# Kernel tuning notes

Hardware: AMD Instinct MI355X
Metric: run time of the kernel (lower is better)

Reference implementation:

```python
import jax, jax.numpy as jnp
import numpy as np
from jax import lax

DETER, STOCH, UNITS, ADIM, EMBED = 4096, 512, 1024, 2, 4096
B, T = 16, 64
ACTION_CLIP = 1.0


def setup_inputs() -> dict:
    key = jax.random.key(0)
    ks = jax.random.split(key, 16)
    s = 0.02
    f32 = jnp.float32
    return {
        "embed": jax.random.normal(ks[0], (B, T, EMBED), f32),
        "action": jax.random.normal(ks[1], (B, T, ADIM), f32),
        "is_first": jax.random.randint(ks[2], (B, T), 0, 2).astype(jnp.int32),
        # learned initial deter state
        "initial_deter": jnp.zeros((DETER,), f32),
        # obs_out: Linear(deter+4096 -> units)
        "w_obs": (jax.random.normal(ks[3], (UNITS, DETER + EMBED), f32) * s),
        "b_obs": jnp.zeros((UNITS,), f32),
        # img_in: Linear(stoch+action_dim -> units)
        "w_imgin": (jax.random.normal(ks[4], (UNITS, STOCH + ADIM), f32) * s),
        "b_imgin": jnp.zeros((UNITS,), f32),
        # img_out: Linear(deter -> units)
        "w_imgout": (jax.random.normal(ks[5], (UNITS, DETER), f32) * s),
        "b_imgout": jnp.zeros((UNITS,), f32),
        # GRUCell params (torch layout: [3*hidden, in] with r,z,n gate order)
        "w_ih": (jax.random.normal(ks[6], (3 * DETER, UNITS), f32) * s),
        "w_hh": (jax.random.normal(ks[7], (3 * DETER, DETER), f32) * s),
        "b_ih": jnp.zeros((3 * DETER,), f32),
        "b_hh": jnp.zeros((3 * DETER,), f32),
        # reparameterization noise for prior/post rsample at each step
        "eps_prior": jax.random.normal(ks[8], (T, B, STOCH), f32),
        "eps_post": jax.random.normal(ks[9], (T, B, STOCH), f32),
    }


def _stats(x):
    mean, std = jnp.split(x, 2, axis=-1)
    std = 2.0 * jax.nn.sigmoid(std / 2.0) + 0.1
    return mean, jnp.maximum(std, 1e-4)  # clamp from get_dist


def _gru(x, h, w_ih, w_hh, b_ih, b_hh):
    gi = x @ w_ih.T + b_ih  # [B, 3*deter]
    gh = h @ w_hh.T + b_hh
    ir, iz, inn = jnp.split(gi, 3, axis=-1)
    hr, hz, hn = jnp.split(gh, 3, axis=-1)
    r = jax.nn.sigmoid(ir + hr)
    z = jax.nn.sigmoid(iz + hz)
    n = jnp.tanh(inn + r * hn)
    return (1.0 - z) * n + z * h


def reference(embed, action, is_first, initial_deter, w_obs, b_obs,
              w_imgin, b_imgin, w_imgout, b_imgout,
              w_ih, w_hh, b_ih, b_hh, eps_prior, eps_post):
    bsz = action.shape[0]
    # initial_state (learned)
    deter0 = jnp.broadcast_to(jnp.tanh(initial_deter)[None, :], (bsz, DETER))
    m0, _ = _stats(deter0 @ w_imgout.T + b_imgout)
    stoch0 = m0  # dist.mean

    def step(carry, xs):
        deter, stoch = carry
        a, emb, first, ep, eo = xs  # [B,A], [B,E], [B], [B,S], [B,S]
        # action clip
        a = a * (ACTION_CLIP / jnp.maximum(jnp.abs(a), ACTION_CLIP))
        mask = (1.0 - first.astype(jnp.float32))[:, None]
        deter_m = deter * mask
        stoch_m = stoch * mask
        a = a * mask
        # img_step
        x = jnp.concatenate([stoch_m, a], axis=-1) @ w_imgin.T + b_imgin
        d_new = _gru(x, deter_m, w_ih, w_hh, b_ih, b_hh)
        pmean, pstd = _stats(d_new @ w_imgout.T + b_imgout)
        pstoch = pmean + pstd * ep
        # obs part
        z = jnp.concatenate([d_new, emb], axis=-1) @ w_obs.T + b_obs
        omean, ostd = _stats(z)
        ostoch = omean + ostd * eo
        out = jnp.concatenate(
            [ostoch, omean, ostd, d_new, pstoch, pmean, pstd, d_new], axis=-1)
        return (d_new, ostoch), out

    xs = (jnp.swapaxes(action, 0, 1), jnp.swapaxes(embed, 0, 1),
          jnp.swapaxes(is_first, 0, 1), eps_prior, eps_post)
    _, outs = lax.scan(step, (deter0, stoch0), xs)  # [T, B, F]
    return jnp.swapaxes(outs, 0, 1)  # [B, T, F]
```

## Files before the change

### kernel.cpp

```cpp
#include <hip/hip_runtime.h>
#include <math.h>

#define B_ 16
#define T_ 64
#define DETER_ 4096
#define STOCH_ 512
#define UNITS_ 1024
#define EMBED_ 4096
#define FOUT_ 11264

enum { JOB_IMGIN=0, JOB_GATES=1, JOB_PRIOR=2, JOB_OBS=3, JOB_PRIOR_INIT=4 };

struct SP {
  const float* embed; const float* action; const int* is_first;
  const float* wpad_imgin; const float* b_imgin;
  const float* w_ih; const float* w_hh; const float* b_ih; const float* b_hh;
  const float* w_imgout; const float* b_imgout;
  const float* w_obs; const float* b_obs;
  const float* eps_prior; const float* eps_post;
  const float* deter_m_in;
  float*       deter_m_out;
  float*       dnew;
  float* stoch_m; float* x_img; float* out;
  int t;
};

__device__ __forceinline__ float4 ld4(const float* p){ return *reinterpret_cast<const float4*>(p); }
__device__ __forceinline__ float sigm(float x){ return 1.f/(1.f+expf(-x)); }
__device__ __forceinline__ float dot4(float4 w, float4 x, float a){
  return fmaf(w.x,x.x, fmaf(w.y,x.y, fmaf(w.z,x.z, fmaf(w.w,x.w, a))));
}

__device__ __forceinline__ void g2l16(const float* g, float* l) {
  __builtin_amdgcn_global_load_lds(
      (const __attribute__((address_space(1))) unsigned int*)g,
      (__attribute__((address_space(3))) unsigned int*)l, 16, 0, 0);
}

__global__ __launch_bounds__(512,4) void gates_pipe(SP p) {
  __shared__ float Xs[16384];
  const int bid = blockIdx.x;
  const int tid = threadIdx.x;
  const int wave = tid>>6, lane = tid&63;
  const int half = lane>>5, sl = lane&31;
  const int t = p.t;
  const int j = bid*8 + wave;
  float* buf0 = Xs; float* buf1 = Xs + 8192;

  float ar[8], az[8], anx[8], anh[8];
  #pragma unroll
  for (int b=0;b<8;++b){ ar[b]=0.f; az[b]=0.f; anx[b]=0.f; anh[b]=0.f; }

  auto stage = [&](float* dst, int c) {
    #pragma unroll
    for (int q=0;q<2;++q) {
      const int b = wave*2+q;
      const float* src = (c<2) ? (p.x_img + b*UNITS_ + c*512)
                               : (p.deter_m_in + b*DETER_ + (c-2)*512);
      g2l16(src + lane*4,       dst + b*512);
      g2l16(src + 256 + lane*4, dst + b*512 + 256);
    }
  };

#define GINNER(AN)                                                      \
  _Pragma("unroll")                                                     \
  for (int it=0; it<4; ++it) {                                          \
    const int k0 = it*128 + sl*4;                                       \
    float4 w_r = ld4(wr+k0), w_z = ld4(wz+k0), w_n = ld4(wn+k0);        \
    _Pragma("unroll")                                                   \
    for (int b=0;b<8;++b) {                                             \
      float4 xv = ld4(cur + (half*8+b)*512 + k0);                       \
      ar[b] = dot4(w_r, xv, ar[b]);                                     \
      az[b] = dot4(w_z, xv, az[b]);                                     \
      AN[b] = dot4(w_n, xv, AN[b]);                                     \
    }                                                                   \
  }

  stage(buf0, 0);
  for (int c=0;c<10;++c) {
    float* cur = (c&1)? buf1 : buf0;
    float* nxt = (c&1)? buf0 : buf1;
    __builtin_amdgcn_s_barrier();
    __builtin_amdgcn_sched_barrier(0);
    if (c < 9) {
      stage(nxt, c+1);
      __builtin_amdgcn_sched_barrier(0);
      asm volatile("s_waitcnt vmcnt(4)" ::: "memory");
    } else {
      asm volatile("s_waitcnt vmcnt(0)" ::: "memory");
    }
    __builtin_amdgcn_sched_barrier(0);
    __builtin_amdgcn_s_barrier();

    const float *wr, *wz, *wn;
    if (c < 2) {
      const size_t o = (size_t)c*512;
      wr = p.w_ih + (size_t)j*1024 + o;
      wz = p.w_ih + (size_t)(4096+j)*1024 + o;
      wn = p.w_ih + (size_t)(8192+j)*1024 + o;
      GINNER(anx)
    } else {
      const size_t o = (size_t)(c-2)*512;
      wr = p.w_hh + (size_t)j*4096 + o;
      wz = p.w_hh + (size_t)(4096+j)*4096 + o;
      wn = p.w_hh + (size_t)(8192+j)*4096 + o;
      GINNER(anh)
    }
  }
#undef GINNER

  #pragma unroll
  for (int off=1; off<32; off<<=1) {
    #pragma unroll
    for (int b=0;b<8;++b) {
      ar[b]  += __shfl_xor(ar[b],  off);
      az[b]  += __shfl_xor(az[b],  off);
      anx[b] += __shfl_xor(anx[b], off);
      anh[b] += __shfl_xor(anh[b], off);
    }
  }
  if (sl==0) {
    #pragma unroll
    for (int b=0;b<8;++b) {
      buf0[(wave*4+0)*16 + half*8 + b] = ar[b];
      buf0[(wave*4+1)*16 + half*8 + b] = az[b];
      buf0[(wave*4+2)*16 + half*8 + b] = anx[b];
      buf0[(wave*4+3)*16 + half*8 + b] = anh[b];
    }
  }
  __syncthreads();

  if (tid < 128) {
    int u = tid&7, b = tid>>3;
    int jj = bid*8 + u;
    const float* res = Xs;
    float rs = res[(u*4+0)*16+b] + p.b_ih[jj]          + p.b_hh[jj];
    float zs = res[(u*4+1)*16+b] + p.b_ih[DETER_+jj]   + p.b_hh[DETER_+jj];
    float ni = res[(u*4+2)*16+b] + p.b_ih[2*DETER_+jj];
    float nh = res[(u*4+3)*16+b] + p.b_hh[2*DETER_+jj];
    float rg = sigm(rs), zg = sigm(zs);
    float ng = tanhf(ni + rg*nh);
    float hp = p.deter_m_in[b*DETER_+jj];
    float d  = (1.f-zg)*ng + zg*hp;
    p.dnew[b*DETER_+jj] = d;
    int tn = t+1;
    float mb2 = (tn<T_) ? (p.is_first[b*T_+tn] ? 0.f : 1.f) : 0.f;
    p.deter_m_out[b*DETER_+jj] = d*mb2;
    size_t ob = ((size_t)(b*T_+t))*FOUT_;
    p.out[ob+1536+jj] = d;
    p.out[ob+7168+jj] = d;
  }
}

template<int JOB>
__device__ __forceinline__ void pipe_mv(const SP& p, int bid, float* Xs) {
  constexpr int NC = (JOB==JOB_OBS)?16:8;
  const int tid = threadIdx.x;
  const int wave = tid>>6, lane = tid&63;
  const int half = lane>>5, sl = lane&31;
  const int t = p.t;
  float* buf0 = Xs; float* buf1 = Xs + 8192;

  float acc[2][8];
  #pragma unroll
  for (int r=0;r<2;++r)
    #pragma unroll
    for (int b=0;b<8;++b) acc[r][b]=0.f;

  int row0, row1;
  {
    int rl0 = wave*2, rl1 = wave*2+1;
    row0 = (rl0<4)? (bid*4+rl0) : (512 + bid*4 + (rl0-4));
    row1 = (rl1<4)? (bid*4+rl1) : (512 + bid*4 + (rl1-4));
  }

  auto stage = [&](float* dst, int c) {
    #pragma unroll
    for (int q=0;q<4;++q) {
      const int b = wave*4+q;
      const float* src;
      if constexpr (JOB==JOB_PRIOR) src = p.dnew + b*DETER_ + c*512;
      else src = (c<8) ? (p.dnew + b*DETER_ + c*512)
                       : (p.embed + ((size_t)(b*T_+t))*EMBED_ + (c-8)*512);
      g2l16(src + lane*4,       dst + b*512);
      g2l16(src + 256 + lane*4, dst + b*512 + 256);
    }
  };

  stage(buf0, 0);
  for (int c=0;c<NC;++c) {
    float* cur = (c&1)? buf1 : buf0;
    float* nxt = (c&1)? buf0 : buf1;
    __builtin_amdgcn_s_barrier();
    __builtin_amdgcn_sched_barrier(0);
    if (c+1 < NC) {
      stage(nxt, c+1);
      __builtin_amdgcn_sched_barrier(0);
      asm volatile("s_waitcnt vmcnt(8)" ::: "memory");
    } else {
      asm volatile("s_waitcnt vmcnt(0)" ::: "memory");
    }
    __builtin_amdgcn_sched_barrier(0);
    __builtin_amdgcn_s_barrier();

    const float *w0, *w1;
    if constexpr (JOB==JOB_PRIOR) {
      w0 = p.w_imgout + (size_t)row0*4096 + (size_t)c*512;
      w1 = p.w_imgout + (size_t)row1*4096 + (size_t)c*512;
    } else {
      w0 = p.w_obs + (size_t)row0*8192 + (size_t)c*512;
      w1 = p.w_obs + (size_t)row1*8192 + (size_t)c*512;
    }
    #pragma unroll
    for (int it=0; it<4; ++it) {
      const int k0 = it*128 + sl*4;
      float4 wa = ld4(w0+k0), wb2 = ld4(w1+k0);
      #pragma unroll
      for (int b=0;b<8;++b) {
        float4 xv = ld4(cur + (half*8+b)*512 + k0);
        acc[0][b] = dot4(wa,  xv, acc[0][b]);
        acc[1][b] = dot4(wb2, xv, acc[1][b]);
      }
    }
  }

  #pragma unroll
  for (int off=1; off<32; off<<=1)
    #pragma unroll
    for (int r=0;r<2;++r)
      #pragma unroll
      for (int b=0;b<8;++b)
        acc[r][b] += __shfl_xor(acc[r][b], off);
  if (sl==0) {
    #pragma unroll
    for (int r=0;r<2;++r)
      #pragma unroll
      for (int b=0;b<8;++b)
        buf0[(wave*2+r)*16 + half*8 + b] = acc[r][b];
  }
  __syncthreads();
  const float* res = Xs;

  if constexpr (JOB==JOB_PRIOR) {
    if (tid < 64) {
      int rl = tid&3, b = tid>>2;
      int jj = bid*4 + rl;
      float mean = res[rl*16+b]     + p.b_imgout[jj];
      float sr   = res[(rl+4)*16+b] + p.b_imgout[512+jj];
      float sd = 2.f*sigm(sr*0.5f) + 0.1f; sd = fmaxf(sd, 1e-4f);
      float ep = p.eps_prior[((size_t)t*B_+b)*STOCH_ + jj];
      size_t ob = ((size_t)(b*T_+t))*FOUT_;
      p.out[ob+5632+jj] = fmaf(sd, ep, mean);
      p.out[ob+6144+jj] = mean;
      p.out[ob+6656+jj] = sd;
    }
  } else {
    if (tid < 64) {
      int rl = tid&3, b = tid>>2;
      int jj = bid*4 + rl;
      float mean = res[rl*16+b]     + p.b_obs[jj];
      float sr   = res[(rl+4)*16+b] + p.b_obs[512+jj];
      float sd = 2.f*sigm(sr*0.5f) + 0.1f; sd = fmaxf(sd, 1e-4f);
      float eo = p.eps_post[((size_t)t*B_+b)*STOCH_ + jj];
      float ost = fmaf(sd, eo, mean);
      size_t ob = ((size_t)(b*T_+t))*FOUT_;
      p.out[ob+0+jj]    = ost;
      p.out[ob+512+jj]  = mean;
      p.out[ob+1024+jj] = sd;
      int tn = t+1;
      float mb2 = (tn<T_) ? (p.is_first[b*T_+tn] ? 0.f : 1.f) : 0.f;
      p.stoch_m[b*STOCH_+jj] = ost*mb2;
    }
  }
}

__global__ __launch_bounds__(256,2) void post_pipe(SP p) {
  __shared__ float Xs[16384];
  if (blockIdx.x < 128) pipe_mv<JOB_PRIOR>(p, blockIdx.x, Xs);
  else                  pipe_mv<JOB_OBS>(p, blockIdx.x - 128, Xs);
}

template<int JOB>
__device__ __forceinline__ void stage_async(const SP& p, float* Xs, int c,
                                            int wave, int lane, int tid, int t) {
  __syncthreads();
  constexpr int SEGS = (JOB==JOB_IMGIN) ? 2 : 4;
  #pragma unroll
  for (int q=0;q<4;++q) {
    const int b = wave*4+q;
    const float* src;
    if constexpr (JOB==JOB_PRIOR_INIT)
      src = p.dnew + b*DETER_ + c*1024;
    else
      src = p.stoch_m + b*STOCH_;
    float* dst = Xs + b*1024;
    #pragma unroll
    for (int seg=0;seg<SEGS;++seg)
      g2l16(src + seg*256 + lane*4, dst + seg*256);
  }
  if constexpr (JOB==JOB_IMGIN) {
    const int kc = tid*4;
    if (kc >= 512) {
      #pragma unroll
      for (int b=0;b<16;++b) {
        float4 v = make_float4(0.f,0.f,0.f,0.f);
        if (kc == 512) {
          float mb = p.is_first[b*T_+t] ? 0.f : 1.f;
          const float* ap = p.action + (b*T_+t)*2;
          float a0 = ap[0], a1 = ap[1];
          v.x = (a0 / fmaxf(fabsf(a0),1.f))*mb;
          v.y = (a1 / fmaxf(fabsf(a1),1.f))*mb;
        }
        *reinterpret_cast<float4*>(Xs + b*1024 + kc) = v;
      }
    }
  }
  __syncthreads();
}

template<int JOB>
__device__ __forceinline__ void mv_body(const SP& p, int bid, float* Xs) {
  constexpr int KTOT = (JOB==JOB_IMGIN)?1024:4096;
  constexpr int CHUNKS = KTOT/1024;
  const int tid = threadIdx.x;
  const int wave = tid>>6, lane = tid&63;
  const int half = lane>>5, sl = lane&31;
  const int t = p.t;

  float acc[2][8];
  #pragma unroll
  for (int r=0;r<2;++r)
    #pragma unroll
    for (int b=0;b<8;++b) acc[r][b]=0.f;

  int rowIdx[2];
  #pragma unroll
  for (int r=0;r<2;++r) rowIdx[r] = bid*8 + wave*2 + r;

  for (int c=0;c<CHUNKS;++c) {
    stage_async<JOB>(p, Xs, c, wave, lane, tid, t);
    const float* w0; const float* w1;
    if constexpr (JOB==JOB_IMGIN) {
      w0 = p.wpad_imgin + (size_t)rowIdx[0]*1024;
      w1 = p.wpad_imgin + (size_t)rowIdx[1]*1024;
    } else {
      w0 = p.w_imgout + (size_t)rowIdx[0]*4096 + (size_t)c*1024;
      w1 = p.w_imgout + (size_t)rowIdx[1]*4096 + (size_t)c*1024;
    }
    #pragma unroll
    for (int it=0; it<8; ++it) {
      const int k0 = it*128 + sl*4;
      float4 wa = ld4(w0 + k0), wb2 = ld4(w1 + k0);
      #pragma unroll
      for (int b=0;b<8;++b) {
        float4 xv = ld4(Xs + (half*8+b)*1024 + k0);
        acc[0][b] = dot4(wa,  xv, acc[0][b]);
        acc[1][b] = dot4(wb2, xv, acc[1][b]);
      }
    }
  }

  #pragma unroll
  for (int off=1; off<32; off<<=1)
    #pragma unroll
    for (int r=0;r<2;++r)
      #pragma unroll
      for (int b=0;b<8;++b)
        acc[r][b] += __shfl_xor(acc[r][b], off);
  __syncthreads();
  if (sl==0) {
    #pragma unroll
    for (int r=0;r<2;++r)
      #pragma unroll
      for (int b=0;b<8;++b)
        Xs[(wave*2+r)*16 + half*8 + b] = acc[r][b];
  }
  __syncthreads();
  const float* res = Xs;

  if constexpr (JOB==JOB_IMGIN) {
    if (tid < 128) {
      int rl = tid&7, b = tid>>3;
      int row = bid*8 + rl;
      p.x_img[b*UNITS_+row] = res[rl*16+b] + p.b_imgin[row];
    }
  } else {
    if (tid < 128) {
      int rl = tid&7, b = tid>>3;
      int row = bid*8 + rl;
      float mean = res[rl*16+b] + p.b_imgout[row];
      float mb = p.is_first[b*T_+0] ? 0.f : 1.f;
      p.stoch_m[b*STOCH_+row] = mean*mb;
    }
  }
}

template<int JOB>
__global__ __launch_bounds__(256,2) void mv_single(SP p) {
  __shared__ float Xs[16*1024];
  mv_body<JOB>(p, blockIdx.x, Xs);
}

__global__ void pad_imgin_kernel(const float* w, float* wpad) {
  int row = blockIdx.x;
  for (int k=threadIdx.x; k<1024; k+=256)
    wpad[row*1024+k] = (k<514) ? w[row*514+k] : 0.f;
}

__global__ void init_deter_kernel(const float* ini, float* det, float* detm,
                                  const int* is_first) {
  int k = blockIdx.x*256 + threadIdx.x;
  float v = tanhf(ini[k]);
  #pragma unroll
  for (int b=0;b<16;++b) {
    det[b*DETER_+k] = v;
    float mb = is_first[b*T_+0] ? 0.f : 1.f;
    detm[b*DETER_+k] = v*mb;
  }
}

extern "C" void kernel_launch(void* const* d_in, const int* in_sizes, int n_in,
                              void* d_out, int out_size, void* d_ws, size_t ws_size,
                              hipStream_t stream) {
  (void)in_sizes; (void)n_in; (void)out_size; (void)ws_size;
  SP p;
  p.embed     = (const float*)d_in[0];
  p.action    = (const float*)d_in[1];
  p.is_first  = (const int*)  d_in[2];
  const float* initial_deter = (const float*)d_in[3];
  p.w_obs     = (const float*)d_in[4];
  p.b_obs     = (const float*)d_in[5];
  const float* w_imgin       = (const float*)d_in[6];
  p.b_imgin   = (const float*)d_in[7];
  p.w_imgout  = (const float*)d_in[8];
  p.b_imgout  = (const float*)d_in[9];
  p.w_ih      = (const float*)d_in[10];
  p.w_hh      = (const float*)d_in[11];
  p.b_ih      = (const float*)d_in[12];
  p.b_hh      = (const float*)d_in[13];
  p.eps_prior = (const float*)d_in[14];
  p.eps_post  = (const float*)d_in[15];
  p.out = (float*)d_out;

  float* ws      = (float*)d_ws;
  float* wpad    = ws;
  float* dnew    = wpad    + 1024*1024;
  float* deterM0 = dnew    + 16*DETER_;
  float* deterM1 = deterM0 + 16*DETER_;
  float* stochm  = deterM1 + 16*DETER_;
  float* ximg    = stochm  + 16*STOCH_;
  p.wpad_imgin = wpad;
  p.stoch_m = stochm;
  p.x_img = ximg;

  pad_imgin_kernel<<<1024,256,0,stream>>>(w_imgin, wpad);
  init_deter_kernel<<<DETER_/256,256,0,stream>>>(initial_deter, dnew, deterM0, p.is_first);

  p.t = 0; p.dnew = dnew; p.deter_m_in = deterM0; p.deter_m_out = deterM1;
  mv_single<JOB_PRIOR_INIT><<<64,256,0,stream>>>(p);

  for (int t=0; t<T_; ++t) {
    p.t = t;
    p.deter_m_in  = (t&1) ? deterM1 : deterM0;
    p.deter_m_out = (t&1) ? deterM0 : deterM1;
    p.dnew        = dnew;
    mv_single<JOB_IMGIN><<<128,256,0,stream>>>(p);
    gates_pipe<<<512,512,0,stream>>>(p);
    post_pipe<<<256,256,0,stream>>>(p);
  }
}
```

Baseline: 11.35 ms.

## Replace LDS-staged pipelined matvecs with direct-load kernels computing two rows per wave

The GRU gate and post-projection kernels no longer stage activations through double-buffered LDS with global_load_lds and barriers. Each wave now reads activations directly from global memory (relying on cache) and computes two output rows per wave, so one activation load feeds more weights. Block counts and thread counts are halved (512x256 for gates, 128 blocks for post). The aim is to drop barrier and staging overhead in these weight-bandwidth-bound matvecs, at the cost of fewer waves in flight and heavier register use, which could reduce the ability to hide memory latency.

```diff
diff --git a/kernel.cpp b/kernel.cpp
--- a/kernel.cpp
+++ b/kernel.cpp
@@ -9,7 +9,7 @@
 #define EMBED_ 4096
 #define FOUT_ 11264
 
-enum { JOB_IMGIN=0, JOB_GATES=1, JOB_PRIOR=2, JOB_OBS=3, JOB_PRIOR_INIT=4 };
+enum { JOB_IMGIN=0, JOB_PRIOR_INIT=4 };
 
 struct SP {
   const float* embed; const float* action; const int* is_first;
@@ -31,113 +31,113 @@
   return fmaf(w.x,x.x, fmaf(w.y,x.y, fmaf(w.z,x.z, fmaf(w.w,x.w, a))));
 }
 
-__device__ __forceinline__ void g2l16(const float* g, float* l) {
-  __builtin_amdgcn_global_load_lds(
-      (const __attribute__((address_space(1))) unsigned int*)g,
-      (__attribute__((address_space(3))) unsigned int*)l, 16, 0, 0);
-}
-
-__global__ __launch_bounds__(512,4) void gates_pipe(SP p) {
-  __shared__ float Xs[16384];
+__global__ __launch_bounds__(256,2) void gates_nb(SP p) {
+  __shared__ float Ls[4*1024 + 8*64];
   const int bid = blockIdx.x;
   const int tid = threadIdx.x;
   const int wave = tid>>6, lane = tid&63;
   const int half = lane>>5, sl = lane&31;
   const int t = p.t;
-  const int j = bid*8 + wave;
-  float* buf0 = Xs; float* buf1 = Xs + 8192;
-
-  float ar[8], az[8], anx[8], anh[8];
-  #pragma unroll
-  for (int b=0;b<8;++b){ ar[b]=0.f; az[b]=0.f; anx[b]=0.f; anh[b]=0.f; }
-
-  auto stage = [&](float* dst, int c) {
-    #pragma unroll
-    for (int q=0;q<2;++q) {
-      const int b = wave*2+q;
-      const float* src = (c<2) ? (p.x_img + b*UNITS_ + c*512)
-                               : (p.deter_m_in + b*DETER_ + (c-2)*512);
-      g2l16(src + lane*4,       dst + b*512);
-      g2l16(src + 256 + lane*4, dst + b*512 + 256);
-    }
-  };
-
-#define GINNER(AN)                                                      \
-  _Pragma("unroll")                                                     \
-  for (int it=0; it<4; ++it) {                                          \
-    const int k0 = it*128 + sl*4;                                       \
-    float4 w_r = ld4(wr+k0), w_z = ld4(wz+k0), w_n = ld4(wn+k0);        \
-    _Pragma("unroll")                                                   \
-    for (int b=0;b<8;++b) {                                             \
-      float4 xv = ld4(cur + (half*8+b)*512 + k0);                       \
-      ar[b] = dot4(w_r, xv, ar[b]);                                     \
-      az[b] = dot4(w_z, xv, az[b]);                                     \
-      AN[b] = dot4(w_n, xv, AN[b]);                                     \
-    }                                                                   \
-  }
-
-  stage(buf0, 0);
-  for (int c=0;c<10;++c) {
-    float* cur = (c&1)? buf1 : buf0;
-    float* nxt = (c&1)? buf0 : buf1;
-    __builtin_amdgcn_s_barrier();
-    __builtin_amdgcn_sched_barrier(0);
-    if (c < 9) {
-      stage(nxt, c+1);
-      __builtin_amdgcn_sched_barrier(0);
-      asm volatile("s_waitcnt vmcnt(4)" ::: "memory");
-    } else {
-      asm volatile("s_waitcnt vmcnt(0)" ::: "memory");
-    }
-    __builtin_amdgcn_sched_barrier(0);
-    __builtin_amdgcn_s_barrier();
-
-    const float *wr, *wz, *wn;
-    if (c < 2) {
-      const size_t o = (size_t)c*512;
-      wr = p.w_ih + (size_t)j*1024 + o;
-      wz = p.w_ih + (size_t)(4096+j)*1024 + o;
-      wn = p.w_ih + (size_t)(8192+j)*1024 + o;
-      GINNER(anx)
-    } else {
-      const size_t o = (size_t)(c-2)*512;
-      wr = p.w_hh + (size_t)j*4096 + o;
-      wz = p.w_hh + (size_t)(4096+j)*4096 + o;
-      wn = p.w_hh + (size_t)(8192+j)*4096 + o;
-      GINNER(anh)
-    }
-  }
-#undef GINNER
-
+  const int j0 = bid*8 + wave*2;
+
+  float ar[2][8], az[2][8], an[2][8];
+  #pragma unroll
+  for (int u=0;u<2;++u)
+    #pragma unroll
+    for (int b=0;b<8;++b){ ar[u][b]=0.f; az[u][b]=0.f; an[u][b]=0.f; }
+
+  for (int kb=0; kb<2; ++kb) {
+    #pragma unroll
+    for (int it=0; it<4; ++it) {
+      const int k0 = kb*512 + it*128 + sl*4;
+      float4 w[2][3];
+      #pragma unroll
+      for (int u=0;u<2;++u)
+        #pragma unroll
+        for (int g=0;g<3;++g)
+          w[u][g] = ld4(p.w_ih + (size_t)(g*4096 + j0+u)*1024 + k0);
+      #pragma unroll
+      for (int b=0;b<8;++b) {
+        float4 xv = ld4(p.x_img + (half*8+b)*UNITS_ + k0);
+        #pragma unroll
+        for (int u=0;u<2;++u) {
+          ar[u][b] = dot4(w[u][0], xv, ar[u][b]);
+          az[u][b] = dot4(w[u][1], xv, az[u][b]);
+          an[u][b] = dot4(w[u][2], xv, an[u][b]);
+        }
+      }
+    }
+  }
+  #pragma unroll
+  for (int u=0;u<2;++u)
+    #pragma unroll
+    for (int b=0;b<8;++b) {
+      Ls[wave*1024 + (u*8+b)*64 + lane] = an[u][b];
+      an[u][b] = 0.f;
+    }
+
+  for (int kb=0; kb<8; ++kb) {
+    #pragma unroll
+    for (int it=0; it<4; ++it) {
+      const int k0 = kb*512 + it*128 + sl*4;
+      float4 w[2][3];
+      #pragma unroll
+      for (int u=0;u<2;++u)
+        #pragma unroll
+        for (int g=0;g<3;++g)
+          w[u][g] = ld4(p.w_hh + (size_t)(g*4096 + j0+u)*4096 + k0);
+      #pragma unroll
+      for (int b=0;b<8;++b) {
+        float4 xv = ld4(p.deter_m_in + (half*8+b)*DETER_ + k0);
+        #pragma unroll
+        for (int u=0;u<2;++u) {
+          ar[u][b] = dot4(w[u][0], xv, ar[u][b]);
+          az[u][b] = dot4(w[u][1], xv, az[u][b]);
+          an[u][b] = dot4(w[u][2], xv, an[u][b]);
+        }
+      }
+    }
+  }
+
+  float anx[2][8];
+  #pragma unroll
+  for (int u=0;u<2;++u)
+    #pragma unroll
+    for (int b=0;b<8;++b)
+      anx[u][b] = Ls[wave*1024 + (u*8+b)*64 + lane];
   #pragma unroll
   for (int off=1; off<32; off<<=1) {
     #pragma unroll
-    for (int b=0;b<8;++b) {
-      ar[b]  += __shfl_xor(ar[b],  off);
-      az[b]  += __shfl_xor(az[b],  off);
-      anx[b] += __shfl_xor(anx[b], off);
-      anh[b] += __shfl_xor(anh[b], off);
-    }
-  }
+    for (int u=0;u<2;++u)
+      #pragma unroll
+      for (int b=0;b<8;++b) {
+        ar[u][b]  += __shfl_xor(ar[u][b],  off);
+        az[u][b]  += __shfl_xor(az[u][b],  off);
+        an[u][b]  += __shfl_xor(an[u][b],  off);
+        anx[u][b] += __shfl_xor(anx[u][b], off);
+      }
+  }
+  float* res = Ls + 4*1024;
   if (sl==0) {
     #pragma unroll
-    for (int b=0;b<8;++b) {
-      buf0[(wave*4+0)*16 + half*8 + b] = ar[b];
-      buf0[(wave*4+1)*16 + half*8 + b] = az[b];
-      buf0[(wave*4+2)*16 + half*8 + b] = anx[b];
-      buf0[(wave*4+3)*16 + half*8 + b] = anh[b];
-    }
+    for (int u=0;u<2;++u)
+      #pragma unroll
+      for (int b=0;b<8;++b) {
+        res[(wave*2+u)*64 + 0*16 + half*8+b] = ar[u][b];
+        res[(wave*2+u)*64 + 1*16 + half*8+b] = az[u][b];
+        res[(wave*2+u)*64 + 2*16 + half*8+b] = anx[u][b];
+        res[(wave*2+u)*64 + 3*16 + half*8+b] = an[u][b];
+      }
   }
   __syncthreads();
 
   if (tid < 128) {
     int u = tid&7, b = tid>>3;
     int jj = bid*8 + u;
-    const float* res = Xs;
-    float rs = res[(u*4+0)*16+b] + p.b_ih[jj]          + p.b_hh[jj];
-    float zs = res[(u*4+1)*16+b] + p.b_ih[DETER_+jj]   + p.b_hh[DETER_+jj];
-    float ni = res[(u*4+2)*16+b] + p.b_ih[2*DETER_+jj];
-    float nh = res[(u*4+3)*16+b] + p.b_hh[2*DETER_+jj];
+    float rs = res[u*64+ 0+b] + p.b_ih[jj]          + p.b_hh[jj];
+    float zs = res[u*64+16+b] + p.b_ih[DETER_+jj]   + p.b_hh[DETER_+jj];
+    float ni = res[u*64+32+b] + p.b_ih[2*DETER_+jj];
+    float nh = res[u*64+48+b] + p.b_hh[2*DETER_+jj];
     float rg = sigm(rs), zg = sigm(zs);
     float ng = tanhf(ni + rg*nh);
     float hp = p.deter_m_in[b*DETER_+jj];
@@ -152,74 +152,47 @@
   }
 }
 
-template<int JOB>
-__device__ __forceinline__ void pipe_mv(const SP& p, int bid, float* Xs) {
-  constexpr int NC = (JOB==JOB_OBS)?16:8;
+template<int OBS>
+__device__ __forceinline__ void post_body(const SP& p, int bid, float* Ls) {
   const int tid = threadIdx.x;
   const int wave = tid>>6, lane = tid&63;
   const int half = lane>>5, sl = lane&31;
   const int t = p.t;
-  float* buf0 = Xs; float* buf1 = Xs + 8192;
-
-  float acc[2][8];
-  #pragma unroll
-  for (int r=0;r<2;++r)
-    #pragma unroll
-    for (int b=0;b<8;++b) acc[r][b]=0.f;
-
-  int row0, row1;
-  {
-    int rl0 = wave*2, rl1 = wave*2+1;
-    row0 = (rl0<4)? (bid*4+rl0) : (512 + bid*4 + (rl0-4));
-    row1 = (rl1<4)? (bid*4+rl1) : (512 + bid*4 + (rl1-4));
-  }
-
-  auto stage = [&](float* dst, int c) {
-    #pragma unroll
-    for (int q=0;q<4;++q) {
-      const int b = wave*4+q;
-      const float* src;
-      if constexpr (JOB==JOB_PRIOR) src = p.dnew + b*DETER_ + c*512;
-      else src = (c<8) ? (p.dnew + b*DETER_ + c*512)
-                       : (p.embed + ((size_t)(b*T_+t))*EMBED_ + (c-8)*512);
-      g2l16(src + lane*4,       dst + b*512);
-      g2l16(src + 256 + lane*4, dst + b*512 + 256);
-    }
-  };
-
-  stage(buf0, 0);
-  for (int c=0;c<NC;++c) {
-    float* cur = (c&1)? buf1 : buf0;
-    float* nxt = (c&1)? buf0 : buf1;
-    __builtin_amdgcn_s_barrier();
-    __builtin_amdgcn_sched_barrier(0);
-    if (c+1 < NC) {
-      stage(nxt, c+1);
-      __builtin_amdgcn_sched_barrier(0);
-      asm volatile("s_waitcnt vmcnt(8)" ::: "memory");
-    } else {
-      asm volatile("s_waitcnt vmcnt(0)" ::: "memory");
-    }
-    __builtin_amdgcn_sched_barrier(0);
-    __builtin_amdgcn_s_barrier();
-
-    const float *w0, *w1;
-    if constexpr (JOB==JOB_PRIOR) {
-      w0 = p.w_imgout + (size_t)row0*4096 + (size_t)c*512;
-      w1 = p.w_imgout + (size_t)row1*4096 + (size_t)c*512;
-    } else {
-      w0 = p.w_obs + (size_t)row0*8192 + (size_t)c*512;
-      w1 = p.w_obs + (size_t)row1*8192 + (size_t)c*512;
-    }
+  const int j0 = bid*8 + wave*2;
+  constexpr int KB = OBS ? 16 : 8;
+
+  float acc[2][2][8];
+  #pragma unroll
+  for (int u=0;u<2;++u)
+    #pragma unroll
+    for (int r=0;r<2;++r)
+      #pragma unroll
+      for (int b=0;b<8;++b) acc[u][r][b]=0.f;
+
+  for (int kb=0; kb<KB; ++kb) {
+    const int useE = OBS && (kb>=8);
     #pragma unroll
     for (int it=0; it<4; ++it) {
-      const int k0 = it*128 + sl*4;
-      float4 wa = ld4(w0+k0), wb2 = ld4(w1+k0);
-      #pragma unroll
-      for (int b=0;b<8;++b) {
-        float4 xv = ld4(cur + (half*8+b)*512 + k0);
-        acc[0][b] = dot4(wa,  xv, acc[0][b]);
-        acc[1][b] = dot4(wb2, xv, acc[1][b]);
+      const int k0 = kb*512 + it*128 + sl*4;
+      float4 w[2][2];
+      #pragma unroll
+      for (int u=0;u<2;++u)
+        #pragma unroll
+        for (int r=0;r<2;++r) {
+          const int row = r*512 + j0+u;
+          w[u][r] = OBS ? ld4(p.w_obs    + (size_t)row*8192 + k0)
+                        : ld4(p.w_imgout + (size_t)row*4096 + k0);
+        }
+      #pragma unroll
+      for (int b=0;b<8;++b) {
+        const int bb = half*8+b;
+        float4 xv = useE ? ld4(p.embed + ((size_t)(bb*T_+t))*EMBED_ + (k0-4096))
+                         : ld4(p.dnew + bb*DETER_ + k0);
+        #pragma unroll
+        for (int u=0;u<2;++u) {
+          acc[u][0][b] = dot4(w[u][0], xv, acc[u][0][b]);
+          acc[u][1][b] = dot4(w[u][1], xv, acc[u][1][b]);
+        }
       }
     }
   }
@@ -227,39 +200,40 @@
   #pragma unroll
   for (int off=1; off<32; off<<=1)
     #pragma unroll
-    for (int r=0;r<2;++r)
-      #pragma unroll
-      for (int b=0;b<8;++b)
-        acc[r][b] += __shfl_xor(acc[r][b], off);
+    for (int u=0;u<2;++u)
+      #pragma unroll
+      for (int r=0;r<2;++r)
+        #pragma unroll
+        for (int b=0;b<8;++b)
+          acc[u][r][b] += __shfl_xor(acc[u][r][b], off);
+
+  float* res = Ls;
   if (sl==0) {
     #pragma unroll
-    for (int r=0;r<2;++r)
-      #pragma unroll
-      for (int b=0;b<8;++b)
-        buf0[(wave*2+r)*16 + half*8 + b] = acc[r][b];
-  }
-  __syncthreads();
-  const float* res = Xs;
-
-  if constexpr (JOB==JOB_PRIOR) {
-    if (tid < 64) {
-      int rl = tid&3, b = tid>>2;
-      int jj = bid*4 + rl;
-      float mean = res[rl*16+b]     + p.b_imgout[jj];
-      float sr   = res[(rl+4)*16+b] + p.b_imgout[512+jj];
+    for (int u=0;u<2;++u)
+      #pragma unroll
+      for (int r=0;r<2;++r)
+        #pragma unroll
+        for (int b=0;b<8;++b)
+          res[(wave*2+u)*32 + r*16 + half*8+b] = acc[u][r][b];
+  }
+  __syncthreads();
+
+  if (tid < 128) {
+    int u = tid&7, b = tid>>3;
+    int jj = bid*8 + u;
+    if constexpr (!OBS) {
+      float mean = res[u*32+ 0+b] + p.b_imgout[jj];
+      float sr   = res[u*32+16+b] + p.b_imgout[512+jj];
       float sd = 2.f*sigm(sr*0.5f) + 0.1f; sd = fmaxf(sd, 1e-4f);
       float ep = p.eps_prior[((size_t)t*B_+b)*STOCH_ + jj];
       size_t ob = ((size_t)(b*T_+t))*FOUT_;
       p.out[ob+5632+jj] = fmaf(sd, ep, mean);
       p.out[ob+6144+jj] = mean;
       p.out[ob+6656+jj] = sd;
-    }
-  } else {
-    if (tid < 64) {
-      int rl = tid&3, b = tid>>2;
-      int jj = bid*4 + rl;
-      float mean = res[rl*16+b]     + p.b_obs[jj];
-      float sr   = res[(rl+4)*16+b] + p.b_obs[512+jj];
+    } else {
+      float mean = res[u*32+ 0+b] + p.b_obs[jj];
+      float sr   = res[u*32+16+b] + p.b_obs[512+jj];
       float sd = 2.f*sigm(sr*0.5f) + 0.1f; sd = fmaxf(sd, 1e-4f);
       float eo = p.eps_post[((size_t)t*B_+b)*STOCH_ + jj];
       float ost = fmaf(sd, eo, mean);
@@ -274,10 +248,16 @@
   }
 }
 
-__global__ __launch_bounds__(256,2) void post_pipe(SP p) {
-  __shared__ float Xs[16384];
-  if (blockIdx.x < 128) pipe_mv<JOB_PRIOR>(p, blockIdx.x, Xs);
-  else                  pipe_mv<JOB_OBS>(p, blockIdx.x - 128, Xs);
+__global__ __launch_bounds__(256,2) void post_nb(SP p) {
+  __shared__ float Ls[8*32];
+  if (blockIdx.x < 64) post_body<0>(p, blockIdx.x, Ls);
+  else                 post_body<1>(p, blockIdx.x - 64, Ls);
+}
+
+__device__ __forceinline__ void g2l16(const float* g, float* l) {
+  __builtin_amdgcn_global_load_lds(
+      (const __attribute__((address_space(1))) unsigned int*)g,
+      (__attribute__((address_space(3))) unsigned int*)l, 16, 0, 0);
 }
 
 template<int JOB>
@@ -465,7 +445,7 @@
     p.deter_m_out = (t&1) ? deterM0 : deterM1;
     p.dnew        = dnew;
     mv_single<JOB_IMGIN><<<128,256,0,stream>>>(p);
-    gates_pipe<<<512,512,0,stream>>>(p);
-    post_pipe<<<256,256,0,stream>>>(p);
-  }
-}
+    gates_nb<<<512,256,0,stream>>>(p);
+    post_nb<<<128,256,0,stream>>>(p);
+  }
+}
```

Measured after the change: 18.16 ms. 60.0% more time.
